# Kernel optimization log

Hardware: AMD Instinct MI355X
Metric: run time of the kernel (lower is better)

The kernel has to match this reference:

```python
import jax, jax.numpy as jnp
import numpy as np

N_NODES = 100000
D = 256            # in_channels
H = 256            # hidden_channels
E = 1000000        # number of query pairs


def setup_inputs() -> dict:
    key = jax.random.key(0)
    ks = jax.random.split(key, 8)
    x = jax.random.normal(ks[0], (N_NODES, D), dtype=jnp.float32)
    edge_index = jax.random.randint(ks[1], (2, 1000), 0, N_NODES, dtype=jnp.int64)
    edge_pairs = jax.random.randint(ks[2], (E, 2), 0, N_NODES, dtype=jnp.int64)
    # MLP params (Linear stores y = x @ W + b, W shaped [in, out])
    s1 = 1.0 / np.sqrt(D)
    s2 = 1.0 / np.sqrt(H)
    s3 = 1.0 / np.sqrt(H // 2)
    W1 = jax.random.uniform(ks[3], (D, H), jnp.float32, -s1, s1)
    b1 = jnp.zeros((H,), jnp.float32)
    W2 = jax.random.uniform(ks[4], (H, H // 2), jnp.float32, -s2, s2)
    b2 = jnp.zeros((H // 2,), jnp.float32)
    W3 = jax.random.uniform(ks[5], (H // 2, 1), jnp.float32, -s3, s3)
    b3 = jnp.zeros((1,), jnp.float32)
    return {"x": x, "W1": W1, "b1": b1, "W2": W2, "b2": b2,
            "W3": W3, "b3": b3, "edge_index": edge_index, "edge_pairs": edge_pairs}


def reference(x, W1, b1, W2, b2, W3, b3, edge_index, edge_pairs):
    # Gather node pairs and form elementwise-product pair features [E, D]
    feats = x[edge_pairs[:, 0]] * x[edge_pairs[:, 1]]
    # 3-layer MLP (dropout inactive at inference)
    h = jax.nn.relu(feats @ W1 + b1)
    h = jax.nn.relu(h @ W2 + b2)
    scores = h @ W3 + b3
    return scores.reshape(-1)
```

## Files before the change

### kernel.cpp

```cpp
#include <hip/hip_runtime.h>


typedef __attribute__((ext_vector_type(8))) short short8;
typedef __attribute__((ext_vector_type(4))) float floatx4;
typedef __attribute__((ext_vector_type(4))) unsigned uintx4;
typedef __attribute__((ext_vector_type(2))) int intx2;

#define MT 64
#define NTHREADS 1024
#define NBLOCKS 512

__device__ __forceinline__ unsigned short f2bf(float f) {
  union { float f; unsigned u; } a; a.f = f;
  unsigned r = a.u + 0x7FFFu + ((a.u >> 16) & 1u);
  return (unsigned short)(r >> 16);
}

__device__ __forceinline__ unsigned bf16mul2(unsigned ua, unsigned ub) {
  float lo = __uint_as_float(ua << 16)          * __uint_as_float(ub << 16);
  float hi = __uint_as_float(ua & 0xFFFF0000u) * __uint_as_float(ub & 0xFFFF0000u);
  return (unsigned)f2bf(lo) | ((unsigned)f2bf(hi) << 16);
}

__global__ void cast_x_kernel(const float* __restrict__ x, unsigned short* __restrict__ xb, int n4) {
  int i = blockIdx.x * blockDim.x + threadIdx.x;
  if (i >= n4) return;
  float4 v = ((const float4*)x)[i];
  ushort4 o;
  o.x = f2bf(v.x); o.y = f2bf(v.y); o.z = f2bf(v.z); o.w = f2bf(v.w);
  ((ushort4*)xb)[i] = o;
}

__global__ void prep_w_kernel(const float* __restrict__ W1, const float* __restrict__ W2,
                              unsigned short* __restrict__ w1t, unsigned short* __restrict__ w2t) {
  int i = blockIdx.x * blockDim.x + threadIdx.x;
  if (i < 256 * 256) {
    int k = i >> 8, n = i & 255;
    w1t[n * 256 + k] = f2bf(W1[k * 256 + n]);
  } else {
    int j = i - 256 * 256;
    if (j < 128 * 256) {
      int k = j >> 7, n = j & 127;
      w2t[n * 256 + k] = f2bf(W2[k * 128 + n]);
    }
  }
}

__global__ void init_out_kernel(float* __restrict__ out, const float* __restrict__ b3, int E) {
  int i = blockIdx.x * blockDim.x + threadIdx.x;
  if (i < E) out[i] = b3[0];
}

__global__ __launch_bounds__(NTHREADS, 4) void mlp_kernel(
    const unsigned short* __restrict__ xb,
    const unsigned short* __restrict__ w1t,
    const unsigned short* __restrict__ w2t,
    const float* __restrict__ b1,
    const float* __restrict__ b2,
    const float* __restrict__ w3,
    const int* __restrict__ ep,
    float* __restrict__ out,
    int E)
{
  __shared__ __align__(16) unsigned short buf[2][MT * 256];

  const int tid  = threadIdx.x;
  const int wv   = tid >> 6;
  const int lane = tid & 63;
  const int q    = lane >> 4;
  const int r16  = lane & 15;
  const int c    = tid & 31;
  const int mr0  = tid >> 5;

  const int ntiles = (E + MT - 1) / MT;

  {
    int t0 = blockIdx.x;
    #pragma unroll
    for (int s = 0; s < 2; ++s) {
      int m = mr0 + 32 * s;
      int g = t0 * MT + m; if (g >= E) g = E - 1;
      intx2 uv = __builtin_nontemporal_load((const intx2*)(ep + 2 * (size_t)g));
      uintx4 a = __builtin_nontemporal_load((const uintx4*)(xb + ((size_t)uv.x << 8) + (c << 3)));
      uintx4 b = __builtin_nontemporal_load((const uintx4*)(xb + ((size_t)uv.y << 8) + (c << 3)));
      uintx4 pv;
      #pragma unroll
      for (int tt = 0; tt < 4; ++tt) pv[tt] = bf16mul2(a[tt], b[tt]);
      *(uintx4*)((char*)buf[0] + m * 512 + ((c ^ (m & 15)) << 4)) = pv;
    }
  }
  __syncthreads();

  int p = 0;
  for (int t = blockIdx.x; t < ntiles; t += NBLOCKS) {
    char* const bufp = (char*)buf[p];
    char* const bufn = (char*)buf[p ^ 1];
    const int tn = (t + NBLOCKS < ntiles) ? (t + NBLOCKS) : t;

    intx2 uvn[2];
    #pragma unroll
    for (int s = 0; s < 2; ++s) {
      int g = tn * MT + mr0 + 32 * s; if (g >= E) g = E - 1;
      uvn[s] = __builtin_nontemporal_load((const intx2*)(ep + 2 * (size_t)g));
    }

    const unsigned short* const b1p = w1t + (wv * 16 + r16) * 256 + q * 8;
    short8 bv1[8];
    #pragma unroll
    for (int kt = 0; kt < 8; ++kt) bv1[kt] = *(const short8*)(b1p + kt * 32);

    floatx4 acc[4];
    #pragma unroll
    for (int i = 0; i < 4; ++i) acc[i] = (floatx4){0.f, 0.f, 0.f, 0.f};

    char* const a1base = bufp + r16 * 512;
    #pragma unroll
    for (int kt = 0; kt < 8; ++kt) {
      const int aoff = (kt << 6) ^ ((q ^ r16) << 4);
      short8 av[4];
      #pragma unroll
      for (int mt = 0; mt < 4; ++mt)
        av[mt] = *(const short8*)(a1base + mt * (16 * 512) + aoff);
      #pragma unroll
      for (int mt = 0; mt < 4; ++mt)
        acc[mt] = __builtin_amdgcn_mfma_f32_16x16x32_bf16(av[mt], bv1[kt], acc[mt], 0, 0, 0);
    }
    __syncthreads();

    {
      const int n1 = wv * 16 + r16;
      const float bias1 = b1[n1];
      #pragma unroll
      for (int mt = 0; mt < 4; ++mt) {
        #pragma unroll
        for (int r = 0; r < 4; ++r) {
          int m = mt * 16 + q * 4 + r;
          float h = fmaxf(acc[mt][r] + bias1, 0.f);
          int ch = (n1 >> 3) ^ (m & 15);
          *(unsigned short*)(bufp + m * 512 + (ch << 4) + ((n1 & 7) << 1)) = f2bf(h);
        }
      }
    }
    __syncthreads();

    const int mg2 = wv >> 3;
    const int ng2 = wv & 7;
    const unsigned short* const b2p = w2t + (ng2 * 16 + r16) * 256 + q * 8;
    short8 bv2[8];
    #pragma unroll
    for (int kt = 0; kt < 8; ++kt) bv2[kt] = *(const short8*)(b2p + kt * 32);

    uintx4 ra[2], rb[2];
    #pragma unroll
    for (int s = 0; s < 2; ++s) {
      ra[s] = __builtin_nontemporal_load((const uintx4*)(xb + ((size_t)uvn[s].x << 8) + (c << 3)));
      rb[s] = __builtin_nontemporal_load((const uintx4*)(xb + ((size_t)uvn[s].y << 8) + (c << 3)));
    }

    floatx4 acc2[2];
    acc2[0] = (floatx4){0.f, 0.f, 0.f, 0.f};
    acc2[1] = (floatx4){0.f, 0.f, 0.f, 0.f};
    char* const a2base = bufp + (mg2 * 32 + r16) * 512;
    #pragma unroll
    for (int kt = 0; kt < 8; ++kt) {
      const int aoff = (kt << 6) ^ ((q ^ r16) << 4);
      short8 av0 = *(const short8*)(a2base + aoff);
      short8 av1 = *(const short8*)(a2base + 16 * 512 + aoff);
      acc2[0] = __builtin_amdgcn_mfma_f32_16x16x32_bf16(av0, bv2[kt], acc2[0], 0, 0, 0);
      acc2[1] = __builtin_amdgcn_mfma_f32_16x16x32_bf16(av1, bv2[kt], acc2[1], 0, 0, 0);
    }

    {
      const int n2 = ng2 * 16 + r16;
      const float b2v = b2[n2];
      const float w3v = w3[n2];
      #pragma unroll
      for (int mt = 0; mt < 2; ++mt) {
        #pragma unroll
        for (int r = 0; r < 4; ++r) {
          float h = fmaxf(acc2[mt][r] + b2v, 0.f);
          float pp = h * w3v;
          pp += __shfl_xor(pp, 1);
          pp += __shfl_xor(pp, 2);
          pp += __shfl_xor(pp, 4);
          pp += __shfl_xor(pp, 8);
          if (r16 == 0) {
            int g = t * MT + mg2 * 32 + mt * 16 + q * 4 + r;
            if (g < E) atomicAdd(out + g, pp);
          }
        }
      }
    }

    #pragma unroll
    for (int s = 0; s < 2; ++s) {
      int m = mr0 + 32 * s;
      uintx4 pv;
      #pragma unroll
      for (int tt = 0; tt < 4; ++tt) pv[tt] = bf16mul2(ra[s][tt], rb[s][tt]);
      *(uintx4*)(bufn + m * 512 + ((c ^ (m & 15)) << 4)) = pv;
    }
    __syncthreads();
    p ^= 1;
  }
}

extern "C" void kernel_launch(void* const* d_in, const int* in_sizes, int n_in,
                              void* d_out, int out_size, void* d_ws, size_t ws_size,
                              hipStream_t stream) {
  const float* x  = (const float*)d_in[0];
  const float* W1 = (const float*)d_in[1];
  const float* b1 = (const float*)d_in[2];
  const float* W2 = (const float*)d_in[3];
  const float* b2 = (const float*)d_in[4];
  const float* W3 = (const float*)d_in[5];
  const float* b3 = (const float*)d_in[6];
  const int*   ep = (const int*)d_in[8];
  float* out = (float*)d_out;

  const int NX = in_sizes[0];
  const int E  = in_sizes[8] / 2;

  unsigned short* xb  = (unsigned short*)d_ws;
  unsigned short* w1t = (unsigned short*)((char*)d_ws + (size_t)NX * 2);
  unsigned short* w2t = w1t + 256 * 256;

  init_out_kernel<<<(E + 255) / 256, 256, 0, stream>>>(out, b3, E);
  cast_x_kernel<<<(NX / 4 + 255) / 256, 256, 0, stream>>>(x, xb, NX / 4);
  prep_w_kernel<<<(256 * 256 + 128 * 256 + 255) / 256, 256, 0, stream>>>(W1, W2, w1t, w2t);
  mlp_kernel<<<NBLOCKS, NTHREADS, 0, stream>>>(xb, w1t, w2t, b1, b2, W3, ep, out, E);
}
```

Baseline: 522.8 us.

## Single-buffer LDS tile and load weights per k-step to raise occupancy

Drops the double-buffered LDS tile and keeps one 32 KB buffer, adding an extra barrier before the next tile's pair features are written. Weight fragments are now loaded per k-iteration instead of being preloaded into register arrays, and the next-tile gathers are issued after the layer-2 MFMAs. The launch bound asks for 8 waves per SIMD, so more workgroups can be resident per CU. In exchange, gather latency overlaps less with compute and each tile pays one more block-wide sync.

```diff
diff --git a/kernel.cpp b/kernel.cpp
--- a/kernel.cpp
+++ b/kernel.cpp
@@ -51,7 +51,7 @@
   if (i < E) out[i] = b3[0];
 }
 
-__global__ __launch_bounds__(NTHREADS, 4) void mlp_kernel(
+__global__ __launch_bounds__(NTHREADS, 8) void mlp_kernel(
     const unsigned short* __restrict__ xb,
     const unsigned short* __restrict__ w1t,
     const unsigned short* __restrict__ w2t,
@@ -62,7 +62,8 @@
     float* __restrict__ out,
     int E)
 {
-  __shared__ __align__(16) unsigned short buf[2][MT * 256];
+  __shared__ __align__(16) unsigned short buf[MT * 256];
+  char* const ldsb = (char*)buf;
 
   const int tid  = threadIdx.x;
   const int wv   = tid >> 6;
@@ -86,15 +87,12 @@
       uintx4 pv;
       #pragma unroll
       for (int tt = 0; tt < 4; ++tt) pv[tt] = bf16mul2(a[tt], b[tt]);
-      *(uintx4*)((char*)buf[0] + m * 512 + ((c ^ (m & 15)) << 4)) = pv;
+      *(uintx4*)(ldsb + m * 512 + ((c ^ (m & 15)) << 4)) = pv;
     }
   }
   __syncthreads();
 
-  int p = 0;
   for (int t = blockIdx.x; t < ntiles; t += NBLOCKS) {
-    char* const bufp = (char*)buf[p];
-    char* const bufn = (char*)buf[p ^ 1];
     const int tn = (t + NBLOCKS < ntiles) ? (t + NBLOCKS) : t;
 
     intx2 uvn[2];
@@ -105,25 +103,22 @@
     }
 
     const unsigned short* const b1p = w1t + (wv * 16 + r16) * 256 + q * 8;
-    short8 bv1[8];
-    #pragma unroll
-    for (int kt = 0; kt < 8; ++kt) bv1[kt] = *(const short8*)(b1p + kt * 32);
-
     floatx4 acc[4];
     #pragma unroll
     for (int i = 0; i < 4; ++i) acc[i] = (floatx4){0.f, 0.f, 0.f, 0.f};
 
-    char* const a1base = bufp + r16 * 512;
+    char* const a1base = ldsb + r16 * 512;
     #pragma unroll
     for (int kt = 0; kt < 8; ++kt) {
       const int aoff = (kt << 6) ^ ((q ^ r16) << 4);
+      short8 bv1 = *(const short8*)(b1p + kt * 32);
       short8 av[4];
       #pragma unroll
       for (int mt = 0; mt < 4; ++mt)
         av[mt] = *(const short8*)(a1base + mt * (16 * 512) + aoff);
       #pragma unroll
       for (int mt = 0; mt < 4; ++mt)
-        acc[mt] = __builtin_amdgcn_mfma_f32_16x16x32_bf16(av[mt], bv1[kt], acc[mt], 0, 0, 0);
+        acc[mt] = __builtin_amdgcn_mfma_f32_16x16x32_bf16(av[mt], bv1, acc[mt], 0, 0, 0);
     }
     __syncthreads();
 
@@ -137,7 +132,7 @@
           int m = mt * 16 + q * 4 + r;
           float h = fmaxf(acc[mt][r] + bias1, 0.f);
           int ch = (n1 >> 3) ^ (m & 15);
-          *(unsigned short*)(bufp + m * 512 + (ch << 4) + ((n1 & 7) << 1)) = f2bf(h);
+          *(unsigned short*)(ldsb + m * 512 + (ch << 4) + ((n1 & 7) << 1)) = f2bf(h);
         }
       }
     }
@@ -146,28 +141,25 @@
     const int mg2 = wv >> 3;
     const int ng2 = wv & 7;
     const unsigned short* const b2p = w2t + (ng2 * 16 + r16) * 256 + q * 8;
-    short8 bv2[8];
-    #pragma unroll
-    for (int kt = 0; kt < 8; ++kt) bv2[kt] = *(const short8*)(b2p + kt * 32);
-
-    uintx4 ra[2], rb[2];
-    #pragma unroll
-    for (int s = 0; s < 2; ++s) {
-      ra[s] = __builtin_nontemporal_load((const uintx4*)(xb + ((size_t)uvn[s].x << 8) + (c << 3)));
-      rb[s] = __builtin_nontemporal_load((const uintx4*)(xb + ((size_t)uvn[s].y << 8) + (c << 3)));
-    }
-
     floatx4 acc2[2];
     acc2[0] = (floatx4){0.f, 0.f, 0.f, 0.f};
     acc2[1] = (floatx4){0.f, 0.f, 0.f, 0.f};
-    char* const a2base = bufp + (mg2 * 32 + r16) * 512;
+    char* const a2base = ldsb + (mg2 * 32 + r16) * 512;
     #pragma unroll
     for (int kt = 0; kt < 8; ++kt) {
       const int aoff = (kt << 6) ^ ((q ^ r16) << 4);
+      short8 bv2 = *(const short8*)(b2p + kt * 32);
       short8 av0 = *(const short8*)(a2base + aoff);
       short8 av1 = *(const short8*)(a2base + 16 * 512 + aoff);
-      acc2[0] = __builtin_amdgcn_mfma_f32_16x16x32_bf16(av0, bv2[kt], acc2[0], 0, 0, 0);
-      acc2[1] = __builtin_amdgcn_mfma_f32_16x16x32_bf16(av1, bv2[kt], acc2[1], 0, 0, 0);
+      acc2[0] = __builtin_amdgcn_mfma_f32_16x16x32_bf16(av0, bv2, acc2[0], 0, 0, 0);
+      acc2[1] = __builtin_amdgcn_mfma_f32_16x16x32_bf16(av1, bv2, acc2[1], 0, 0, 0);
+    }
+
+    uintx4 ra[2], rb[2];
+    #pragma unroll
+    for (int s = 0; s < 2; ++s) {
+      ra[s] = __builtin_nontemporal_load((const uintx4*)(xb + ((size_t)uvn[s].x << 8) + (c << 3)));
+      rb[s] = __builtin_nontemporal_load((const uintx4*)(xb + ((size_t)uvn[s].y << 8) + (c << 3)));
     }
 
     {
@@ -191,6 +183,7 @@
         }
       }
     }
+    __syncthreads();
 
     #pragma unroll
     for (int s = 0; s < 2; ++s) {
@@ -198,10 +191,9 @@
       uintx4 pv;
       #pragma unroll
       for (int tt = 0; tt < 4; ++tt) pv[tt] = bf16mul2(ra[s][tt], rb[s][tt]);
-      *(uintx4*)(bufn + m * 512 + ((c ^ (m & 15)) << 4)) = pv;
-    }
-    __syncthreads();
-    p ^= 1;
+      *(uintx4*)(ldsb + m * 512 + ((c ^ (m & 15)) << 4)) = pv;
+    }
+    __syncthreads();
   }
 }
 
```

Result: slower. 899.3 us (+72.0%).

## Double tile rows and reduce layer-3 scores in LDS instead of global atomics

Applied to the files above, without the earlier changes.

The row tile grows from 64 to 128 pair rows and the block count is halved. Each wave now reuses its register-held W1/W2 fragments across twice as many MFMA row tiles. The final dot products are summed through shared-memory atomics and written once per row with the b3 bias added, so the init kernel and the many global atomicAdds go away. The cost is twice the LDS footprint and more live accumulator registers, which likely allows only one 1024-thread block per CU.

```diff
diff --git a/kernel.cpp b/kernel.cpp
--- a/kernel.cpp
+++ b/kernel.cpp
@@ -6,9 +6,9 @@
 typedef __attribute__((ext_vector_type(4))) unsigned uintx4;
 typedef __attribute__((ext_vector_type(2))) int intx2;
 
-#define MT 64
+#define MT 128
 #define NTHREADS 1024
-#define NBLOCKS 512
+#define NBLOCKS 256
 
 __device__ __forceinline__ unsigned short f2bf(float f) {
   union { float f; unsigned u; } a; a.f = f;
@@ -46,11 +46,6 @@
   }
 }
 
-__global__ void init_out_kernel(float* __restrict__ out, const float* __restrict__ b3, int E) {
-  int i = blockIdx.x * blockDim.x + threadIdx.x;
-  if (i < E) out[i] = b3[0];
-}
-
 __global__ __launch_bounds__(NTHREADS, 4) void mlp_kernel(
     const unsigned short* __restrict__ xb,
     const unsigned short* __restrict__ w1t,
@@ -58,11 +53,13 @@
     const float* __restrict__ b1,
     const float* __restrict__ b2,
     const float* __restrict__ w3,
+    const float* __restrict__ b3,
     const int* __restrict__ ep,
     float* __restrict__ out,
     int E)
 {
   __shared__ __align__(16) unsigned short buf[2][MT * 256];
+  __shared__ float ss[MT];
 
   const int tid  = threadIdx.x;
   const int wv   = tid >> 6;
@@ -71,13 +68,17 @@
   const int r16  = lane & 15;
   const int c    = tid & 31;
   const int mr0  = tid >> 5;
+  const int swz16 = (q ^ r16) << 4;
 
   const int ntiles = (E + MT - 1) / MT;
+  const float b3v = b3[0];
+
+  if (tid < MT) ss[tid] = 0.f;
 
   {
     int t0 = blockIdx.x;
     #pragma unroll
-    for (int s = 0; s < 2; ++s) {
+    for (int s = 0; s < 4; ++s) {
       int m = mr0 + 32 * s;
       int g = t0 * MT + m; if (g >= E) g = E - 1;
       intx2 uv = __builtin_nontemporal_load((const intx2*)(ep + 2 * (size_t)g));
@@ -97,9 +98,9 @@
     char* const bufn = (char*)buf[p ^ 1];
     const int tn = (t + NBLOCKS < ntiles) ? (t + NBLOCKS) : t;
 
-    intx2 uvn[2];
-    #pragma unroll
-    for (int s = 0; s < 2; ++s) {
+    intx2 uvn[4];
+    #pragma unroll
+    for (int s = 0; s < 4; ++s) {
       int g = tn * MT + mr0 + 32 * s; if (g >= E) g = E - 1;
       uvn[s] = __builtin_nontemporal_load((const intx2*)(ep + 2 * (size_t)g));
     }
@@ -109,20 +110,20 @@
     #pragma unroll
     for (int kt = 0; kt < 8; ++kt) bv1[kt] = *(const short8*)(b1p + kt * 32);
 
-    floatx4 acc[4];
-    #pragma unroll
-    for (int i = 0; i < 4; ++i) acc[i] = (floatx4){0.f, 0.f, 0.f, 0.f};
+    floatx4 acc[8];
+    #pragma unroll
+    for (int i = 0; i < 8; ++i) acc[i] = (floatx4){0.f, 0.f, 0.f, 0.f};
 
     char* const a1base = bufp + r16 * 512;
     #pragma unroll
     for (int kt = 0; kt < 8; ++kt) {
-      const int aoff = (kt << 6) ^ ((q ^ r16) << 4);
-      short8 av[4];
-      #pragma unroll
-      for (int mt = 0; mt < 4; ++mt)
+      const int aoff = (kt << 6) ^ swz16;
+      short8 av[8];
+      #pragma unroll
+      for (int mt = 0; mt < 8; ++mt)
         av[mt] = *(const short8*)(a1base + mt * (16 * 512) + aoff);
       #pragma unroll
-      for (int mt = 0; mt < 4; ++mt)
+      for (int mt = 0; mt < 8; ++mt)
         acc[mt] = __builtin_amdgcn_mfma_f32_16x16x32_bf16(av[mt], bv1[kt], acc[mt], 0, 0, 0);
     }
     __syncthreads();
@@ -131,7 +132,7 @@
       const int n1 = wv * 16 + r16;
       const float bias1 = b1[n1];
       #pragma unroll
-      for (int mt = 0; mt < 4; ++mt) {
+      for (int mt = 0; mt < 8; ++mt) {
         #pragma unroll
         for (int r = 0; r < 4; ++r) {
           int m = mt * 16 + q * 4 + r;
@@ -150,24 +151,27 @@
     #pragma unroll
     for (int kt = 0; kt < 8; ++kt) bv2[kt] = *(const short8*)(b2p + kt * 32);
 
-    uintx4 ra[2], rb[2];
-    #pragma unroll
-    for (int s = 0; s < 2; ++s) {
+    uintx4 ra[4], rb[4];
+    #pragma unroll
+    for (int s = 0; s < 4; ++s) {
       ra[s] = __builtin_nontemporal_load((const uintx4*)(xb + ((size_t)uvn[s].x << 8) + (c << 3)));
       rb[s] = __builtin_nontemporal_load((const uintx4*)(xb + ((size_t)uvn[s].y << 8) + (c << 3)));
     }
 
-    floatx4 acc2[2];
-    acc2[0] = (floatx4){0.f, 0.f, 0.f, 0.f};
-    acc2[1] = (floatx4){0.f, 0.f, 0.f, 0.f};
-    char* const a2base = bufp + (mg2 * 32 + r16) * 512;
+    floatx4 acc2[4];
+    #pragma unroll
+    for (int i = 0; i < 4; ++i) acc2[i] = (floatx4){0.f, 0.f, 0.f, 0.f};
+    char* const a2base = bufp + (mg2 * 64 + r16) * 512;
     #pragma unroll
     for (int kt = 0; kt < 8; ++kt) {
-      const int aoff = (kt << 6) ^ ((q ^ r16) << 4);
-      short8 av0 = *(const short8*)(a2base + aoff);
-      short8 av1 = *(const short8*)(a2base + 16 * 512 + aoff);
-      acc2[0] = __builtin_amdgcn_mfma_f32_16x16x32_bf16(av0, bv2[kt], acc2[0], 0, 0, 0);
-      acc2[1] = __builtin_amdgcn_mfma_f32_16x16x32_bf16(av1, bv2[kt], acc2[1], 0, 0, 0);
+      const int aoff = (kt << 6) ^ swz16;
+      short8 av[4];
+      #pragma unroll
+      for (int mt = 0; mt < 4; ++mt)
+        av[mt] = *(const short8*)(a2base + mt * (16 * 512) + aoff);
+      #pragma unroll
+      for (int mt = 0; mt < 4; ++mt)
+        acc2[mt] = __builtin_amdgcn_mfma_f32_16x16x32_bf16(av[mt], bv2[kt], acc2[mt], 0, 0, 0);
     }
 
     {
@@ -175,7 +179,7 @@
       const float b2v = b2[n2];
       const float w3v = w3[n2];
       #pragma unroll
-      for (int mt = 0; mt < 2; ++mt) {
+      for (int mt = 0; mt < 4; ++mt) {
         #pragma unroll
         for (int r = 0; r < 4; ++r) {
           float h = fmaxf(acc2[mt][r] + b2v, 0.f);
@@ -184,16 +188,14 @@
           pp += __shfl_xor(pp, 2);
           pp += __shfl_xor(pp, 4);
           pp += __shfl_xor(pp, 8);
-          if (r16 == 0) {
-            int g = t * MT + mg2 * 32 + mt * 16 + q * 4 + r;
-            if (g < E) atomicAdd(out + g, pp);
-          }
+          if (r16 == 0)
+            atomicAdd(&ss[mg2 * 64 + mt * 16 + q * 4 + r], pp);
         }
       }
     }
 
     #pragma unroll
-    for (int s = 0; s < 2; ++s) {
+    for (int s = 0; s < 4; ++s) {
       int m = mr0 + 32 * s;
       uintx4 pv;
       #pragma unroll
@@ -201,6 +203,12 @@
       *(uintx4*)(bufn + m * 512 + ((c ^ (m & 15)) << 4)) = pv;
     }
     __syncthreads();
+
+    if (tid < MT) {
+      int g = t * MT + tid;
+      if (g < E) out[g] = ss[tid] + b3v;
+      ss[tid] = 0.f;
+    }
     p ^= 1;
   }
 }
@@ -225,8 +233,7 @@
   unsigned short* w1t = (unsigned short*)((char*)d_ws + (size_t)NX * 2);
   unsigned short* w2t = w1t + 256 * 256;
 
-  init_out_kernel<<<(E + 255) / 256, 256, 0, stream>>>(out, b3, E);
   cast_x_kernel<<<(NX / 4 + 255) / 256, 256, 0, stream>>>(x, xb, NX / 4);
   prep_w_kernel<<<(256 * 256 + 128 * 256 + 255) / 256, 256, 0, stream>>>(W1, W2, w1t, w2t);
-  mlp_kernel<<<NBLOCKS, NTHREADS, 0, stream>>>(xb, w1t, w2t, b1, b2, W3, ep, out, E);
-}
+  mlp_kernel<<<NBLOCKS, NTHREADS, 0, stream>>>(xb, w1t, w2t, b1, b2, W3, b3, ep, out, E);
+}
```

Result: slower. 543.5 us (+4.0%).
